# Kernel tuning notes

Hardware: AMD Instinct MI355X
Metric: run time of the kernel (lower is better)

The kernel has to match this reference:

```python
import jax, jax.numpy as jnp
import numpy as np

TEMP = 0.05
MOMENTUM = 0.2
B, D, P = 1024, 2048, 16384


def setup_inputs() -> dict:
    key = jax.random.key(0)
    k1, k2, k3, k4, k5 = jax.random.split(key, 5)
    input_features = jax.random.normal(k1, (B, D), dtype=jnp.float32)
    storage = jax.random.normal(k2, (P, D), dtype=jnp.float32)
    # storage holds L2-normalized proxy centroids
    storage = storage / jnp.linalg.norm(storage, axis=1, keepdims=True)
    camids = jax.random.randint(k3, (B,), 0, 8, dtype=jnp.int64)
    proxy_labels = jax.random.randint(k4, (B,), 0, 2048, dtype=jnp.int64)
    abs_proxy_labels = jax.random.randint(k5, (B,), 0, P, dtype=jnp.int64)
    return {
        "input_features": input_features,
        "storage": storage,
        "camids": camids,
        "proxy_labels": proxy_labels,
        "abs_proxy_labels": abs_proxy_labels,
    }


def reference(input_features, storage, camids, proxy_labels, abs_proxy_labels):
    # logits = x @ storage^T / temp  (dense GEMM vs proxy memory bank)
    logits = jnp.einsum("bd,pd->bp", input_features, storage) / TEMP
    logp = jax.nn.log_softmax(logits, axis=1)
    # NLL loss (mean reduction) over the true absolute proxy index
    loss = -jnp.mean(logp[jnp.arange(logp.shape[0]), abs_proxy_labels])

    # Sequential per-sample momentum-EMA scatter update + row renorm
    # (duplicate indices compound sequentially, matching the torch loop)
    def step(S, xl):
        x, l = xl
        row = MOMENTUM * S[l] + (1.0 - MOMENTUM) * x
        row = row / jnp.linalg.norm(row)
        return S.at[l].set(row), None

    new_storage, _ = jax.lax.scan(step, storage, (input_features, abs_proxy_labels))
    return loss, new_storage
```

## Files before the change

### kernel.cpp

```cpp
#include <hip/hip_runtime.h>
#include <cmath>

constexpr int B_N = 1024;
constexpr int D_N = 2048;
constexpr int P_N = 16384;
constexpr int TILE = 128;
constexpr int BK = 64;
constexpr int NT = P_N / TILE;
constexpr int NIT = D_N / BK;
#define TEMP_INV 20.0f
#define S_SCALE 16.0f
#define LOGIT_SCALE (TEMP_INV / S_SCALE)
#define MOM 0.2f

typedef __attribute__((ext_vector_type(4))) float floatx4;

__device__ __forceinline__ unsigned int pack4_fp8(float4 v) {
    unsigned int w = __builtin_amdgcn_cvt_pk_fp8_f32(v.x, v.y, 0, false);
    w = __builtin_amdgcn_cvt_pk_fp8_f32(v.z, v.w, w, true);
    return w;
}

__device__ __forceinline__ void gl_lds16(const void* g, void* l) {
    __builtin_amdgcn_global_load_lds(
        (const __attribute__((address_space(1))) void*)g,
        (__attribute__((address_space(3))) void*)l, 16, 0, 0);
}

__device__ __forceinline__ void row_update(
    const float* __restrict__ X, const int* __restrict__ labels,
    int p, int t, float4 v0, float4 v1, float* __restrict__ outS,
    unsigned long long* mask, float* red) {
    if (t < 16) mask[t] = 0ull;
    __syncthreads();
    for (int u = 0; u < 4; ++u) {
        int k = u * 256 + t;
        if (labels[k] == p) atomicOr(&mask[k >> 6], 1ull << (k & 63));
    }
    __syncthreads();
    unsigned long long any = 0;
    for (int w = 0; w < 16; ++w) any |= mask[w];
    float4* o4 = (float4*)(outS + (size_t)p * D_N);
    if (!any) {
        o4[t] = v0; o4[256 + t] = v1;
        return;
    }
    float r[8] = {v0.x, v0.y, v0.z, v0.w, v1.x, v1.y, v1.z, v1.w};
    int k = -1;
    for (int w = 0; w < 16; ++w) {
        if (mask[w]) { k = w * 64 + (int)__builtin_ctzll(mask[w]); break; }
    }
    const int lane = t & 63, wv = t >> 6;
    while (k >= 0) {
        const float4* xk = (const float4*)(X + (size_t)k * D_N);
        float4 a0 = xk[t], a1 = xk[256 + t];
        float ss = 0.f;
        r[0] = MOM * r[0] + (1.f - MOM) * a0.x; ss += r[0] * r[0];
        r[1] = MOM * r[1] + (1.f - MOM) * a0.y; ss += r[1] * r[1];
        r[2] = MOM * r[2] + (1.f - MOM) * a0.z; ss += r[2] * r[2];
        r[3] = MOM * r[3] + (1.f - MOM) * a0.w; ss += r[3] * r[3];
        r[4] = MOM * r[4] + (1.f - MOM) * a1.x; ss += r[4] * r[4];
        r[5] = MOM * r[5] + (1.f - MOM) * a1.y; ss += r[5] * r[5];
        r[6] = MOM * r[6] + (1.f - MOM) * a1.z; ss += r[6] * r[6];
        r[7] = MOM * r[7] + (1.f - MOM) * a1.w; ss += r[7] * r[7];
        for (int off = 32; off; off >>= 1) ss += __shfl_xor(ss, off);
        if (lane == 0) red[wv] = ss;
        __syncthreads();
        ss = red[0] + red[1] + red[2] + red[3];
        __syncthreads();
        float inv = 1.0f / sqrtf(ss);
        for (int u = 0; u < 8; ++u) r[u] *= inv;
        int nk = -1;
        int w0 = k >> 6;
        unsigned long long bb = (mask[w0] >> (k & 63)) >> 1;
        if (bb) nk = k + 1 + (int)__builtin_ctzll(bb);
        else {
            for (int w = w0 + 1; w < 16; ++w) {
                if (mask[w]) { nk = w * 64 + (int)__builtin_ctzll(mask[w]); break; }
            }
        }
        k = nk;
    }
    o4[t] = make_float4(r[0], r[1], r[2], r[3]);
    o4[256 + t] = make_float4(r[4], r[5], r[6], r[7]);
}

__global__ __launch_bounds__(256) void convert_update_kernel(
    const float* __restrict__ X, const float* __restrict__ S,
    unsigned char* __restrict__ Xf8, unsigned char* __restrict__ Sf8,
    float* __restrict__ out0, float* __restrict__ outS,
    const int* __restrict__ labels) {
    const int t = threadIdx.x;
    const int p = blockIdx.x;
    if (p == 0 && t == 0) out0[0] = 0.f;
    if (p >= P_N) {
        const int row = p - P_N;
        const float4* x4 = (const float4*)(X + (size_t)row * D_N);
        unsigned int* q = (unsigned int*)(Xf8 + (size_t)row * D_N);
        q[t] = pack4_fp8(x4[t]);
        q[256 + t] = pack4_fp8(x4[256 + t]);
        return;
    }
    const float4* s4 = (const float4*)(S + (size_t)p * D_N);
    unsigned int* q = (unsigned int*)(Sf8 + (size_t)p * D_N);
    float4 v0 = s4[t], v1 = s4[256 + t];
    float4 w0 = make_float4(v0.x * S_SCALE, v0.y * S_SCALE, v0.z * S_SCALE, v0.w * S_SCALE);
    float4 w1 = make_float4(v1.x * S_SCALE, v1.y * S_SCALE, v1.z * S_SCALE, v1.w * S_SCALE);
    q[t] = pack4_fp8(w0);
    q[256 + t] = pack4_fp8(w1);
    if (outS) {
        __shared__ unsigned long long mask[16];
        __shared__ float red[4];
        row_update(X, labels, p, t, v0, v1, outS, mask, red);
    }
}

__global__ __launch_bounds__(256, 4) void gemm_softmax_kernel(
    const unsigned char* __restrict__ Xf8, const unsigned char* __restrict__ Sf8,
    float* __restrict__ part_max, float* __restrict__ part_sum) {
    __shared__ alignas(16) unsigned char sA[2][TILE * BK];
    __shared__ alignas(16) unsigned char sB[2][TILE * BK];
    __shared__ float pmax[2][TILE];
    __shared__ float psum[2][TILE];

    const int t = threadIdx.x;
    const int b = blockIdx.x;
    const int xcd = b & 7;
    const int s = b >> 3;
    const int bm = s >> 4;
    const int bn = (xcd << 4) | (s & 15);
    const int m0 = bm * TILE;
    const int n0 = bn * TILE;

    const int lane = t & 63;
    const int wave = t >> 6;
    const int wm = (wave & 1) * 64;
    const int wn = (wave >> 1) * 64;
    const int frow = lane & 15;
    const int q = lane >> 4;

    const int r0 = t >> 2, r1 = (t + 256) >> 2;
    const int sc0 = ((t & 3) ^ ((r0 & 3) ^ ((r0 >> 2) & 3))) << 4;
    const int sc1 = ((t & 3) ^ ((r1 & 3) ^ ((r1 >> 2) & 3))) << 4;
    const size_t rowA0 = (size_t)(m0 + r0) * D_N + sc0;
    const size_t rowA1 = (size_t)(m0 + r1) * D_N + sc1;
    const size_t rowB0 = (size_t)(n0 + r0) * D_N + sc0;
    const size_t rowB1 = (size_t)(n0 + r1) * D_N + sc1;

#define STAGE(bi, kt) do { const int kof = (kt) * BK;                 \
        gl_lds16(Xf8 + rowA0 + kof, &sA[bi][t * 16]);                 \
        gl_lds16(Xf8 + rowA1 + kof, &sA[bi][(t + 256) * 16]);         \
        gl_lds16(Sf8 + rowB0 + kof, &sB[bi][t * 16]);                 \
        gl_lds16(Sf8 + rowB1 + kof, &sB[bi][(t + 256) * 16]); } while (0)

    const int gswz = (frow & 3) ^ (frow >> 2);
    const int half = (q & 1) * 8;
    const int l0 = q >> 1;
    const int cof0 = (((l0) ^ gswz) << 4) + half;
    const int cof1 = (((l0 | 2) ^ gswz) << 4) + half;
    int aoffs[4], boffs[4];
#pragma unroll
    for (int i = 0; i < 4; ++i) aoffs[i] = (wm + i * 16 + frow) * BK;
#pragma unroll
    for (int j = 0; j < 4; ++j) boffs[j] = (wn + j * 16 + frow) * BK;

    floatx4 acc[4][4];
#pragma unroll
    for (int i = 0; i < 4; ++i)
#pragma unroll
        for (int j = 0; j < 4; ++j)
            acc[i][j] = floatx4{0.f, 0.f, 0.f, 0.f};

    STAGE(0, 0);
    STAGE(1, 1);
    int cur = 0;
    for (int it = 0; it < NIT; ++it) {
        if (it < NIT - 1) asm volatile("s_waitcnt vmcnt(4)" ::: "memory");
        else              asm volatile("s_waitcnt vmcnt(0)" ::: "memory");
        __builtin_amdgcn_s_barrier();
        const unsigned char* pa = &sA[cur][0];
        const unsigned char* pb = &sB[cur][0];
#pragma unroll
        for (int kk = 0; kk < 2; ++kk) {
            const int cof = kk ? cof1 : cof0;
            long long af[4], bf[4];
#pragma unroll
            for (int i = 0; i < 4; ++i)
                af[i] = *(const long long*)(pa + aoffs[i] + cof);
#pragma unroll
            for (int j = 0; j < 4; ++j)
                bf[j] = *(const long long*)(pb + boffs[j] + cof);
#pragma unroll
            for (int i = 0; i < 4; ++i)
#pragma unroll
                for (int j = 0; j < 4; ++j)
                    acc[i][j] = __builtin_amdgcn_mfma_f32_16x16x32_fp8_fp8(
                        af[i], bf[j], acc[i][j], 0, 0, 0);
        }
        __builtin_amdgcn_sched_barrier(0);
        __builtin_amdgcn_s_barrier();
        if (it + 2 < NIT) STAGE(cur, it + 2);
        cur ^= 1;
    }
#undef STAGE

    float lmax[4][4], lsum[4][4];
    for (int i = 0; i < 4; i++) {
        for (int r = 0; r < 4; r++) {
            float m = -INFINITY;
            for (int j = 0; j < 4; j++) m = fmaxf(m, acc[i][j][r] * LOGIT_SCALE);
            for (int off = 1; off < 16; off <<= 1) m = fmaxf(m, __shfl_xor(m, off));
            float s2 = 0.f;
            for (int j = 0; j < 4; j++) s2 += __expf(acc[i][j][r] * LOGIT_SCALE - m);
            for (int off = 1; off < 16; off <<= 1) s2 += __shfl_xor(s2, off);
            lmax[i][r] = m; lsum[i][r] = s2;
        }
    }
    if ((lane & 15) == 0) {
        int lg = lane >> 4;
        for (int i = 0; i < 4; i++)
            for (int r = 0; r < 4; r++) {
                int row = wm + i * 16 + lg * 4 + r;
                pmax[wave >> 1][row] = lmax[i][r];
                psum[wave >> 1][row] = lsum[i][r];
            }
    }
    __syncthreads();
    if (t < TILE) {
        float ma = pmax[0][t], mb = pmax[1][t];
        float M = fmaxf(ma, mb);
        float Sv = psum[0][t] * __expf(ma - M) + psum[1][t] * __expf(mb - M);
        int grow = m0 + t;
        part_max[(size_t)grow * NT + bn] = M;
        part_sum[(size_t)grow * NT + bn] = Sv;
    }
}

__global__ __launch_bounds__(256) void loss_kernel(
    const float* __restrict__ X, const float* __restrict__ S,
    const int* __restrict__ labels,
    const float* __restrict__ part_max, const float* __restrict__ part_sum,
    float* __restrict__ out0) {
    const int wave = threadIdx.x >> 6, lane = threadIdx.x & 63;
    const int row = blockIdx.x * 4 + wave;
    const float4* x4 = (const float4*)(X + (size_t)row * D_N);
    const float4* s4 = (const float4*)(S + (size_t)labels[row] * D_N);
    float acc = 0.f;
    for (int k = lane; k < D_N / 4; k += 64) {
        float4 a = x4[k], bb = s4[k];
        acc += a.x * bb.x + a.y * bb.y + a.z * bb.z + a.w * bb.w;
    }
    for (int off = 32; off; off >>= 1) acc += __shfl_xor(acc, off);
    float ll = acc * TEMP_INV;
    const float* pm = part_max + (size_t)row * NT;
    const float* ps = part_sum + (size_t)row * NT;
    float m1 = pm[lane], m2 = pm[lane + 64];
    float M = fmaxf(m1, m2);
    for (int off = 32; off; off >>= 1) M = fmaxf(M, __shfl_xor(M, off));
    float Sv = ps[lane] * __expf(m1 - M) + ps[lane + 64] * __expf(m2 - M);
    for (int off = 32; off; off >>= 1) Sv += __shfl_xor(Sv, off);
    float v = ll - (M + __logf(Sv));
    __shared__ float red[4];
    if (lane == 0) red[wave] = v;
    __syncthreads();
    if (threadIdx.x == 0)
        atomicAdd(out0, -(red[0] + red[1] + red[2] + red[3]) * (1.0f / (float)B_N));
}

__global__ __launch_bounds__(256) void update_copy_kernel(
    const float* __restrict__ X, const float* __restrict__ S,
    const int* __restrict__ labels, float* __restrict__ outS) {
    __shared__ unsigned long long mask[16];
    __shared__ float red[4];
    const int p = blockIdx.x;
    const int t = threadIdx.x;
    const float4* s4 = (const float4*)(S + (size_t)p * D_N);
    float4 v0 = s4[t], v1 = s4[256 + t];
    row_update(X, labels, p, t, v0, v1, outS, mask, red);
}

extern "C" void kernel_launch(void* const* d_in, const int* in_sizes, int n_in,
                              void* d_out, int out_size, void* d_ws, size_t ws_size,
                              hipStream_t stream) {
    const float* X = (const float*)d_in[0];
    const float* S = (const float*)d_in[1];
    const int* labels = (const int*)d_in[4];
    float* out = (float*)d_out;

    const size_t sf8_bytes = (size_t)P_N * D_N;
    const size_t xf8_bytes = (size_t)B_N * D_N;
    const size_t need = sf8_bytes + xf8_bytes + (size_t)B_N * NT * 8 + 64;
    const bool use_ws = (ws_size >= need);

    unsigned char* scratch = use_ws ? (unsigned char*)d_ws
                                    : (unsigned char*)d_out + 16;
    unsigned char* Sf8 = scratch;
    unsigned char* Xf8 = scratch + sf8_bytes;
    float* part_max = (float*)(Xf8 + xf8_bytes);
    float* part_sum = part_max + (size_t)B_N * NT;

    convert_update_kernel<<<17408, 256, 0, stream>>>(
        X, S, Xf8, Sf8, out, use_ws ? (out + 1) : nullptr, labels);
    gemm_softmax_kernel<<<1024, 256, 0, stream>>>(Xf8, Sf8, part_max, part_sum);
    loss_kernel<<<256, 256, 0, stream>>>(X, S, labels, part_max, part_sum, out);
    if (!use_ws)
        update_copy_kernel<<<P_N, 256, 0, stream>>>(X, S, labels, out + 1);
}
```

Measured before the change: 317.4 us.

## Split storage copy from sparse label-driven EMA update and fuse label logit

Replaces the per-proxy-row convert+update kernel, which scanned all 1024 labels for each of 16384 rows, with a grid-stride streaming kernel that copies storage, converts it to FP8 and converts X. A separate 1024-block kernel then applies the sequential EMA chain only to labelled rows, using the first occurrence of each label as the owner. That kernel also computes the label logit against the original storage row, so the loss kernel no longer has to redo that dot product. The cost is an extra launch, and the storage copy and its update now run in separate kernels that must stay ordered on the stream.

```diff
diff --git a/kernel.cpp b/kernel.cpp
--- a/kernel.cpp
+++ b/kernel.cpp
@@ -27,48 +27,99 @@
         (__attribute__((address_space(3))) void*)l, 16, 0, 0);
 }
 
-__device__ __forceinline__ void row_update(
-    const float* __restrict__ X, const int* __restrict__ labels,
-    int p, int t, float4 v0, float4 v1, float* __restrict__ outS,
-    unsigned long long* mask, float* red) {
+constexpr int S_F4 = P_N * D_N / 4;
+constexpr int S_ITER = S_F4 / 1024;
+constexpr int X_F4 = B_N * D_N / 4;
+constexpr int X_ITER = X_F4 / 1024;
+constexpr int TOT_ITER = S_ITER + X_ITER;
+
+__global__ __launch_bounds__(256) void stream_convert_kernel(
+    const float* __restrict__ X, const float* __restrict__ S,
+    unsigned char* __restrict__ Xf8, unsigned char* __restrict__ Sf8,
+    float* __restrict__ out0, float* __restrict__ outS) {
+    const int t = threadIdx.x;
+    if (blockIdx.x == 0 && t == 0) out0[0] = 0.f;
+    for (int bi = blockIdx.x; bi < TOT_ITER; bi += gridDim.x) {
+        if (bi < S_ITER) {
+            const size_t base = (size_t)bi * 1024;
+            const float4* s4 = (const float4*)S + base;
+            unsigned int* q = (unsigned int*)Sf8 + base;
+            float4 v[4];
+#pragma unroll
+            for (int j = 0; j < 4; ++j) v[j] = s4[t + j * 256];
+            if (outS) {
+                float4* o4 = (float4*)outS + base;
+#pragma unroll
+                for (int j = 0; j < 4; ++j) o4[t + j * 256] = v[j];
+            }
+#pragma unroll
+            for (int j = 0; j < 4; ++j) {
+                float4 w = make_float4(v[j].x * S_SCALE, v[j].y * S_SCALE,
+                                       v[j].z * S_SCALE, v[j].w * S_SCALE);
+                q[t + j * 256] = pack4_fp8(w);
+            }
+        } else {
+            const size_t base = (size_t)(bi - S_ITER) * 1024;
+            const float4* x4 = (const float4*)X + base;
+            unsigned int* q = (unsigned int*)Xf8 + base;
+#pragma unroll
+            for (int j = 0; j < 4; ++j) q[t + j * 256] = pack4_fp8(x4[t + j * 256]);
+        }
+    }
+}
+
+__global__ __launch_bounds__(256) void update_kernel(
+    const float* __restrict__ X, const float* __restrict__ S,
+    const int* __restrict__ labels, float* __restrict__ outS,
+    float* __restrict__ ll) {
+    __shared__ int sl[B_N];
+    __shared__ unsigned long long mask[16];
+    __shared__ float red[8];
+    __shared__ int s_found;
+    const int j = blockIdx.x;
+    const int t = threadIdx.x;
+    for (int k = t; k < B_N; k += 256) sl[k] = labels[k];
+    if (t == 0) s_found = 0;
     if (t < 16) mask[t] = 0ull;
     __syncthreads();
+    const int l = sl[j];
     for (int u = 0; u < 4; ++u) {
         int k = u * 256 + t;
-        if (labels[k] == p) atomicOr(&mask[k >> 6], 1ull << (k & 63));
-    }
-    __syncthreads();
-    unsigned long long any = 0;
-    for (int w = 0; w < 16; ++w) any |= mask[w];
-    float4* o4 = (float4*)(outS + (size_t)p * D_N);
-    if (!any) {
-        o4[t] = v0; o4[256 + t] = v1;
-        return;
-    }
-    float r[8] = {v0.x, v0.y, v0.z, v0.w, v1.x, v1.y, v1.z, v1.w};
-    int k = -1;
-    for (int w = 0; w < 16; ++w) {
-        if (mask[w]) { k = w * 64 + (int)__builtin_ctzll(mask[w]); break; }
-    }
+        if (k < j && sl[k] == l) s_found = 1;
+        if (k > j && sl[k] == l) atomicOr(&mask[k >> 6], 1ull << (k & 63));
+    }
+    __syncthreads();
+    if (s_found) return;
+
+    const float4* s4 = (const float4*)(S + (size_t)l * D_N);
+    float4 v0 = s4[t], v1 = s4[256 + t];
+    float r[8]  = {v0.x, v0.y, v0.z, v0.w, v1.x, v1.y, v1.z, v1.w};
+    float so[8] = {v0.x, v0.y, v0.z, v0.w, v1.x, v1.y, v1.z, v1.w};
     const int lane = t & 63, wv = t >> 6;
-    while (k >= 0) {
-        const float4* xk = (const float4*)(X + (size_t)k * D_N);
-        float4 a0 = xk[t], a1 = xk[256 + t];
-        float ss = 0.f;
-        r[0] = MOM * r[0] + (1.f - MOM) * a0.x; ss += r[0] * r[0];
-        r[1] = MOM * r[1] + (1.f - MOM) * a0.y; ss += r[1] * r[1];
-        r[2] = MOM * r[2] + (1.f - MOM) * a0.z; ss += r[2] * r[2];
-        r[3] = MOM * r[3] + (1.f - MOM) * a0.w; ss += r[3] * r[3];
-        r[4] = MOM * r[4] + (1.f - MOM) * a1.x; ss += r[4] * r[4];
-        r[5] = MOM * r[5] + (1.f - MOM) * a1.y; ss += r[5] * r[5];
-        r[6] = MOM * r[6] + (1.f - MOM) * a1.z; ss += r[6] * r[6];
-        r[7] = MOM * r[7] + (1.f - MOM) * a1.w; ss += r[7] * r[7];
-        for (int off = 32; off; off >>= 1) ss += __shfl_xor(ss, off);
-        if (lane == 0) red[wv] = ss;
+    int k = j;
+    while (true) {
+        const float4* x4 = (const float4*)(X + (size_t)k * D_N);
+        float4 a0 = x4[t], a1 = x4[256 + t];
+        float xr[8] = {a0.x, a0.y, a0.z, a0.w, a1.x, a1.y, a1.z, a1.w};
+        float ss = 0.f, dt = 0.f;
+#pragma unroll
+        for (int u = 0; u < 8; ++u) {
+            r[u] = MOM * r[u] + (1.f - MOM) * xr[u];
+            ss += r[u] * r[u];
+            dt += so[u] * xr[u];
+        }
+        for (int off = 32; off; off >>= 1) {
+            ss += __shfl_xor(ss, off);
+            dt += __shfl_xor(dt, off);
+        }
+        if (lane == 0) { red[wv] = ss; red[4 + wv] = dt; }
         __syncthreads();
         ss = red[0] + red[1] + red[2] + red[3];
+        dt = red[4] + red[5] + red[6] + red[7];
         __syncthreads();
+        if (t == 0) ll[k] = dt * TEMP_INV;
         float inv = 1.0f / sqrtf(ss);
+#pragma unroll
         for (int u = 0; u < 8; ++u) r[u] *= inv;
         int nk = -1;
         int w0 = k >> 6;
@@ -79,40 +130,81 @@
                 if (mask[w]) { nk = w * 64 + (int)__builtin_ctzll(mask[w]); break; }
             }
         }
+        if (nk < 0) break;
         k = nk;
     }
+    float4* o4 = (float4*)(outS + (size_t)l * D_N);
     o4[t] = make_float4(r[0], r[1], r[2], r[3]);
     o4[256 + t] = make_float4(r[4], r[5], r[6], r[7]);
 }
 
-__global__ __launch_bounds__(256) void convert_update_kernel(
+__device__ __forceinline__ void row_update(
+    const float* __restrict__ X, const int* __restrict__ labels,
+    int p, int t, float4 v0, float4 v1, float* __restrict__ outS,
+    unsigned long long* mask, float* red) {
+    if (t < 16) mask[t] = 0ull;
+    __syncthreads();
+    for (int u = 0; u < 4; ++u) {
+        int k = u * 256 + t;
+        if (labels[k] == p) atomicOr(&mask[k >> 6], 1ull << (k & 63));
+    }
+    __syncthreads();
+    unsigned long long any = 0;
+    for (int w = 0; w < 16; ++w) any |= mask[w];
+    float4* o4 = (float4*)(outS + (size_t)p * D_N);
+    if (!any) {
+        o4[t] = v0; o4[256 + t] = v1;
+        return;
+    }
+    float r[8] = {v0.x, v0.y, v0.z, v0.w, v1.x, v1.y, v1.z, v1.w};
+    int k = -1;
+    for (int w = 0; w < 16; ++w) {
+        if (mask[w]) { k = w * 64 + (int)__builtin_ctzll(mask[w]); break; }
+    }
+    const int lane = t & 63, wv = t >> 6;
+    while (k >= 0) {
+        const float4* xk = (const float4*)(X + (size_t)k * D_N);
+        float4 a0 = xk[t], a1 = xk[256 + t];
+        float xr[8] = {a0.x, a0.y, a0.z, a0.w, a1.x, a1.y, a1.z, a1.w};
+        float ss = 0.f;
+#pragma unroll
+        for (int u = 0; u < 8; ++u) {
+            r[u] = MOM * r[u] + (1.f - MOM) * xr[u];
+            ss += r[u] * r[u];
+        }
+        for (int off = 32; off; off >>= 1) ss += __shfl_xor(ss, off);
+        if (lane == 0) red[wv] = ss;
+        __syncthreads();
+        ss = red[0] + red[1] + red[2] + red[3];
+        __syncthreads();
+        float inv = 1.0f / sqrtf(ss);
+#pragma unroll
+        for (int u = 0; u < 8; ++u) r[u] *= inv;
+        int nk = -1;
+        int w0 = k >> 6;
+        unsigned long long bb = (mask[w0] >> (k & 63)) >> 1;
+        if (bb) nk = k + 1 + (int)__builtin_ctzll(bb);
+        else {
+            for (int w = w0 + 1; w < 16; ++w) {
+                if (mask[w]) { nk = w * 64 + (int)__builtin_ctzll(mask[w]); break; }
+            }
+        }
+        k = nk;
+    }
+    o4[t] = make_float4(r[0], r[1], r[2], r[3]);
+    o4[256 + t] = make_float4(r[4], r[5], r[6], r[7]);
+}
+
+__global__ __launch_bounds__(256) void update_copy_kernel(
     const float* __restrict__ X, const float* __restrict__ S,
-    unsigned char* __restrict__ Xf8, unsigned char* __restrict__ Sf8,
-    float* __restrict__ out0, float* __restrict__ outS,
-    const int* __restrict__ labels) {
+    const int* __restrict__ labels, float* __restrict__ outS) {
+    __shared__ unsigned long long mask[16];
+    __shared__ float red[4];
+    const int p = blockIdx.x;
     const int t = threadIdx.x;
-    const int p = blockIdx.x;
-    if (p == 0 && t == 0) out0[0] = 0.f;
-    if (p >= P_N) {
-        const int row = p - P_N;
-        const float4* x4 = (const float4*)(X + (size_t)row * D_N);
-        unsigned int* q = (unsigned int*)(Xf8 + (size_t)row * D_N);
-        q[t] = pack4_fp8(x4[t]);
-        q[256 + t] = pack4_fp8(x4[256 + t]);
-        return;
-    }
     const float4* s4 = (const float4*)(S + (size_t)p * D_N);
-    unsigned int* q = (unsigned int*)(Sf8 + (size_t)p * D_N);
     float4 v0 = s4[t], v1 = s4[256 + t];
-    float4 w0 = make_float4(v0.x * S_SCALE, v0.y * S_SCALE, v0.z * S_SCALE, v0.w * S_SCALE);
-    float4 w1 = make_float4(v1.x * S_SCALE, v1.y * S_SCALE, v1.z * S_SCALE, v1.w * S_SCALE);
-    q[t] = pack4_fp8(w0);
-    q[256 + t] = pack4_fp8(w1);
-    if (outS) {
-        __shared__ unsigned long long mask[16];
-        __shared__ float red[4];
-        row_update(X, labels, p, t, v0, v1, outS, mask, red);
-    }
+    row_update(X, labels, p, t, v0, v1, outS, mask, red);
 }
 
 __global__ __launch_bounds__(256, 4) void gemm_softmax_kernel(
@@ -240,18 +332,23 @@
     const float* __restrict__ X, const float* __restrict__ S,
     const int* __restrict__ labels,
     const float* __restrict__ part_max, const float* __restrict__ part_sum,
-    float* __restrict__ out0) {
+    const float* __restrict__ ll_in, float* __restrict__ out0) {
     const int wave = threadIdx.x >> 6, lane = threadIdx.x & 63;
     const int row = blockIdx.x * 4 + wave;
-    const float4* x4 = (const float4*)(X + (size_t)row * D_N);
-    const float4* s4 = (const float4*)(S + (size_t)labels[row] * D_N);
-    float acc = 0.f;
-    for (int k = lane; k < D_N / 4; k += 64) {
-        float4 a = x4[k], bb = s4[k];
-        acc += a.x * bb.x + a.y * bb.y + a.z * bb.z + a.w * bb.w;
-    }
-    for (int off = 32; off; off >>= 1) acc += __shfl_xor(acc, off);
-    float ll = acc * TEMP_INV;
+    float ll;
+    if (ll_in) {
+        ll = ll_in[row];
+    } else {
+        const float4* x4 = (const float4*)(X + (size_t)row * D_N);
+        const float4* s4 = (const float4*)(S + (size_t)labels[row] * D_N);
+        float acc = 0.f;
+        for (int k = lane; k < D_N / 4; k += 64) {
+            float4 a = x4[k], bb = s4[k];
+            acc += a.x * bb.x + a.y * bb.y + a.z * bb.z + a.w * bb.w;
+        }
+        for (int off = 32; off; off >>= 1) acc += __shfl_xor(acc, off);
+        ll = acc * TEMP_INV;
+    }
     const float* pm = part_max + (size_t)row * NT;
     const float* ps = part_sum + (size_t)row * NT;
     float m1 = pm[lane], m2 = pm[lane + 64];
@@ -267,18 +364,6 @@
         atomicAdd(out0, -(red[0] + red[1] + red[2] + red[3]) * (1.0f / (float)B_N));
 }
 
-__global__ __launch_bounds__(256) void update_copy_kernel(
-    const float* __restrict__ X, const float* __restrict__ S,
-    const int* __restrict__ labels, float* __restrict__ outS) {
-    __shared__ unsigned long long mask[16];
-    __shared__ float red[4];
-    const int p = blockIdx.x;
-    const int t = threadIdx.x;
-    const float4* s4 = (const float4*)(S + (size_t)p * D_N);
-    float4 v0 = s4[t], v1 = s4[256 + t];
-    row_update(X, labels, p, t, v0, v1, outS, mask, red);
-}
-
 extern "C" void kernel_launch(void* const* d_in, const int* in_sizes, int n_in,
                               void* d_out, int out_size, void* d_ws, size_t ws_size,
                               hipStream_t stream) {
@@ -289,7 +374,8 @@
 
     const size_t sf8_bytes = (size_t)P_N * D_N;
     const size_t xf8_bytes = (size_t)B_N * D_N;
-    const size_t need = sf8_bytes + xf8_bytes + (size_t)B_N * NT * 8 + 64;
+    const size_t need = sf8_bytes + xf8_bytes + (size_t)B_N * NT * 8
+                        + (size_t)B_N * 4 + 64;
     const bool use_ws = (ws_size >= need);
 
     unsigned char* scratch = use_ws ? (unsigned char*)d_ws
@@ -298,11 +384,15 @@
     unsigned char* Xf8 = scratch + sf8_bytes;
     float* part_max = (float*)(Xf8 + xf8_bytes);
     float* part_sum = part_max + (size_t)B_N * NT;
-
-    convert_update_kernel<<<17408, 256, 0, stream>>>(
-        X, S, Xf8, Sf8, out, use_ws ? (out + 1) : nullptr, labels);
+    float* ll = part_sum + (size_t)B_N * NT;
+
+    stream_convert_kernel<<<2048, 256, 0, stream>>>(
+        X, S, Xf8, Sf8, out, use_ws ? (out + 1) : nullptr);
+    if (use_ws)
+        update_kernel<<<B_N, 256, 0, stream>>>(X, S, labels, out + 1, ll);
     gemm_softmax_kernel<<<1024, 256, 0, stream>>>(Xf8, Sf8, part_max, part_sum);
-    loss_kernel<<<256, 256, 0, stream>>>(X, S, labels, part_max, part_sum, out);
+    loss_kernel<<<256, 256, 0, stream>>>(X, S, labels, part_max, part_sum,
+                                         use_ws ? ll : nullptr, out);
     if (!use_ws)
         update_copy_kernel<<<P_N, 256, 0, stream>>>(X, S, labels, out + 1);
 }
```

Result: no change. 322.3 us (+1.6%).
